# Kernel optimization log

Measured on AMD Instinct MI355X. Metric: run time of the kernel, lower is better.

## Reference

```python
import jax, jax.numpy as jnp
import numpy as np

D_MODEL = 512
NUM_HEADS = 8
DEPTH = D_MODEL // NUM_HEADS
NEG_INF = -1e9


def setup_inputs() -> dict:
    key = jax.random.key(0)
    ks = jax.random.split(key, 12)
    B, S = 4, 2048
    scale = 1.0 / np.sqrt(D_MODEL)
    inp = {
        "q": jax.random.normal(ks[0], (B, S, D_MODEL), jnp.float32),
        "k": jax.random.normal(ks[1], (B, S, D_MODEL), jnp.float32),
        "v": jax.random.normal(ks[2], (B, S, D_MODEL), jnp.float32),
        "mask": jnp.zeros((1, 1, S, S), jnp.float32),
        # Dense layer params (keras Dense = x @ W + b)
        "wq": jax.random.normal(ks[3], (D_MODEL, D_MODEL), jnp.float32) * scale,
        "bq": jnp.zeros((D_MODEL,), jnp.float32),
        "wk": jax.random.normal(ks[4], (D_MODEL, D_MODEL), jnp.float32) * scale,
        "bk": jnp.zeros((D_MODEL,), jnp.float32),
        "wv": jax.random.normal(ks[5], (D_MODEL, D_MODEL), jnp.float32) * scale,
        "bv": jnp.zeros((D_MODEL,), jnp.float32),
        "wo": jax.random.normal(ks[6], (D_MODEL, D_MODEL), jnp.float32) * scale,
        "bo": jnp.zeros((D_MODEL,), jnp.float32),
    }
    return inp


def _split_heads(x):
    # [B, S, D] -> [B, H, S, depth]
    B, S, _ = x.shape
    return x.reshape(B, S, NUM_HEADS, DEPTH).transpose(0, 2, 1, 3)


def reference(q, k, v, mask, wq, bq, wk, bk, wv, bv, wo, bo):
    B, S, _ = q.shape
    qh = _split_heads(q @ wq + bq)  # [B,H,S,depth]
    kh = _split_heads(k @ wk + bk)
    vh = _split_heads(v @ wv + bv)
    logits = jnp.einsum("bhqd,bhkd->bhqk", qh, kh) / jnp.sqrt(
        jnp.asarray(DEPTH, qh.dtype)
    )
    logits = logits + mask * NEG_INF
    attn = jax.nn.softmax(logits, axis=-1)
    out = jnp.einsum("bhqk,bhkd->bhqd", attn, vh)  # [B,H,S,depth]
    out = out.transpose(0, 2, 1, 3).reshape(B, S, D_MODEL)
    return out @ wo + bo
```

## Files before the change

### kernel.cpp

```cpp
#include <hip/hip_runtime.h>
#include <hip/hip_bf16.h>

#define S_LEN 2048
#define DM    512
#define NH    8
#define DH    64

typedef float  f4   __attribute__((ext_vector_type(4)));
typedef float  f16v __attribute__((ext_vector_type(16)));
typedef short  s8v  __attribute__((ext_vector_type(8)));
typedef __bf16 b8v  __attribute__((ext_vector_type(8)));
union F8 { s8v s; b8v b; };
union U4 { unsigned u[4]; s8v s; b8v b; };

typedef __attribute__((address_space(1))) const void gas_t;
typedef __attribute__((address_space(3))) void       las_t;

__device__ __forceinline__ void gl16(const void* g, void* l) {
  __builtin_amdgcn_global_load_lds((gas_t*)g, (las_t*)l, 16, 0, 0);
}

__device__ __forceinline__ ushort f2bf(float x) {
  unsigned u = __float_as_uint(x);
  u += 0x7FFFu + ((u >> 16) & 1u);
  return (ushort)(u >> 16);
}
__device__ __forceinline__ unsigned pk2(float a, float b) {
  union { __hip_bfloat162 h; unsigned u; } cv;
  cv.h = __float22bfloat162_rn(make_float2(a, b));
  return cv.u;
}

__device__ __forceinline__ void plswap(unsigned a, unsigned b,
                                       unsigned& lo, unsigned& hi2) {
#if __has_builtin(__builtin_amdgcn_permlane32_swap)
  auto r = __builtin_amdgcn_permlane32_swap((int)a, (int)b, false, false);
  lo  = (unsigned)r[0];
  hi2 = (unsigned)r[1];
#else
  const bool ish = (threadIdx.x & 32) != 0;
  const unsigned sa = (unsigned)__shfl_xor((int)a, 32);
  const unsigned sb = (unsigned)__shfl_xor((int)b, 32);
  lo  = ish ? sb : a;
  hi2 = ish ? b  : sa;
#endif
}

__global__ void mask_scan(const float* __restrict__ m, int* __restrict__ flag) {
  const int i = blockIdx.x * 256 + threadIdx.x;
  const float4 v = ((const float4*)m)[i];
  const bool nz = (v.x != 0.f) | (v.y != 0.f) | (v.z != 0.f) | (v.w != 0.f);
  if (nz) atomicOr(flag, 1);
}

__global__ void cvt3(const float* __restrict__ q, const float* __restrict__ k,
                     const float* __restrict__ v, ushort* __restrict__ oq,
                     ushort* __restrict__ ok, ushort* __restrict__ ov) {
  const int z = blockIdx.y;
  const float* s = (z == 0) ? q : (z == 1) ? k : v;
  ushort* d = (z == 0) ? oq : (z == 1) ? ok : ov;
  const size_t i = ((size_t)blockIdx.x * 256 + threadIdx.x) * 8;
  const float4 a = *(const float4*)(s + i);
  const float4 b = *(const float4*)(s + i + 4);
  s8v r;
  r[0] = (short)f2bf(a.x); r[1] = (short)f2bf(a.y);
  r[2] = (short)f2bf(a.z); r[3] = (short)f2bf(a.w);
  r[4] = (short)f2bf(b.x); r[5] = (short)f2bf(b.y);
  r[6] = (short)f2bf(b.z); r[7] = (short)f2bf(b.w);
  *(s8v*)(d + i) = r;
}

__global__ void wtrans(const float* __restrict__ w0, const float* __restrict__ w1,
                       const float* __restrict__ w2, const float* __restrict__ w3,
                       ushort* __restrict__ o0, ushort* __restrict__ o1,
                       ushort* __restrict__ o2, ushort* __restrict__ o3) {
  const int z = blockIdx.z;
  const float* src = (z == 0) ? w0 : (z == 1) ? w1 : (z == 2) ? w2 : w3;
  ushort* dst = (z == 0) ? o0 : (z == 1) ? o1 : (z == 2) ? o2 : o3;
  __shared__ float tile[32][33];
  const int tx = threadIdx.x, ty = threadIdx.y;
  const int k0 = blockIdx.x * 32, n0 = blockIdx.y * 32;
#pragma unroll
  for (int i = 0; i < 4; ++i)
    tile[ty + i * 8][tx] = src[(size_t)(k0 + ty + i * 8) * DM + n0 + tx];
  __syncthreads();
#pragma unroll
  for (int i = 0; i < 4; ++i)
    dst[(size_t)(n0 + ty + i * 8) * DM + k0 + tx] = f2bf(tile[tx][ty + i * 8]);
}

__device__ __forceinline__ void gemm_core(
    const ushort* __restrict__ A, const ushort* __restrict__ Bt,
    const float* __restrict__ bias, void* __restrict__ out, int mode,
    ushort* As, ushort* Bs) {
  const int tid  = threadIdx.x;
  const int lane = tid & 63, wave = tid >> 6;
  const int ql = lane & 15, lg = lane >> 4;
  const int wr = wave >> 1, wc = wave & 1;
  const int tm = blockIdx.x, tn = blockIdx.y;

  const int srow  = wave * 32 + (lane >> 2);
  const int sbyte = (lane & 3) * 16;

  const char* gA = (const char*)(A  + (size_t)(tm * 128 + srow) * 512) + sbyte;
  const char* gB = (const char*)(Bt + (size_t)(tn * 128 + srow) * 512) + sbyte;
  char* lA = (char*)As + wave * 2048;
  char* lB = (char*)Bs + wave * 2048;

  f4 acc[4][4] = {};

  for (int kt = 0; kt < 16; ++kt) {
    const size_t gofs = (size_t)kt * 64;
    gl16(gA + gofs, lA);
    gl16(gA + gofs + 16 * 512 * 2, lA + 1024);
    gl16(gB + gofs, lB);
    gl16(gB + gofs + 16 * 512 * 2, lB + 1024);
    __syncthreads();
    F8 af[4], bf[4];
#pragma unroll
    for (int i = 0; i < 4; ++i) {
      af[i].s = *(const s8v*)(As + (wr * 64 + i * 16 + ql) * 32 + lg * 8);
      bf[i].s = *(const s8v*)(Bs + (wc * 64 + i * 16 + ql) * 32 + lg * 8);
    }
#pragma unroll
    for (int i = 0; i < 4; ++i)
#pragma unroll
      for (int j = 0; j < 4; ++j)
        acc[i][j] = __builtin_amdgcn_mfma_f32_16x16x32_bf16(af[i].b, bf[j].b,
                                                            acc[i][j], 0, 0, 0);
    __syncthreads();
  }

#pragma unroll
  for (int i = 0; i < 4; ++i) {
#pragma unroll
    for (int j = 0; j < 4; ++j) {
      const int n = tn * 128 + wc * 64 + j * 16 + ql;
      const float bz = bias[n];
#pragma unroll
      for (int r = 0; r < 4; ++r) {
        const int m = tm * 128 + wr * 64 + i * 16 + lg * 4 + r;
        const float val = acc[i][j][r] + bz;
        if (mode == 2) {
          ((float*)out)[(size_t)m * DM + n] = val;
        } else {
          const int b = m >> 11, s = m & 2047, h = n >> 6, d = n & 63;
          if (mode == 0)
            ((ushort*)out)[((size_t)(b * NH + h) * S_LEN + s) * DH + d] = f2bf(val);
          else
            ((ushort*)out)[((size_t)(b * NH + h) * DH + d) * S_LEN + s] = f2bf(val);
        }
      }
    }
  }
}

__global__ __launch_bounds__(256) void gemm_qkv(
    const ushort* __restrict__ Xq, const ushort* __restrict__ Xk,
    const ushort* __restrict__ Xv, const ushort* __restrict__ Wtq,
    const ushort* __restrict__ Wtk, const ushort* __restrict__ Wtv,
    const float* __restrict__ bq, const float* __restrict__ bk,
    const float* __restrict__ bv, ushort* __restrict__ Qh,
    ushort* __restrict__ Kh, ushort* __restrict__ Vt) {
  __shared__ ushort As[128 * 32], Bs[128 * 32];
  const int z = blockIdx.z;
  const ushort* A  = (z == 0) ? Xq : (z == 1) ? Xk : Xv;
  const ushort* Bp = (z == 0) ? Wtq : (z == 1) ? Wtk : Wtv;
  const float* bias = (z == 0) ? bq : (z == 1) ? bk : bv;
  void* out = (z == 0) ? (void*)Qh : (z == 1) ? (void*)Kh : (void*)Vt;
  gemm_core(A, Bp, bias, out, (z == 2) ? 1 : 0, As, Bs);
}

__global__ __launch_bounds__(256) void gemm_o(
    const ushort* __restrict__ Obf, const ushort* __restrict__ Wto,
    const float* __restrict__ bo, float* __restrict__ out) {
  __shared__ ushort As[128 * 32], Bs[128 * 32];
  gemm_core(Obf, Wto, bo, out, 2, As, Bs);
}

__global__ __launch_bounds__(256, 2) void attn(
    const ushort* __restrict__ Qh, const ushort* __restrict__ Kh,
    const ushort* __restrict__ Vt, const float* __restrict__ mask,
    const int* __restrict__ flagp, ushort* __restrict__ Obf) {
  __shared__ ushort Ks[2][4096];
  __shared__ ushort Vs[2][4096];

  const float K2 = 0.18033688011f;
  const float C2 = 17.3123404907f;

  const int bid = (blockIdx.x & 7) * 64 + (blockIdx.x >> 3);
  const int bh = bid >> 4, qb = bid & 15;
  const int tid = threadIdx.x, lane = tid & 63, wave = tid >> 6;
  const int cl = lane & 31, hi = lane >> 5;
  const int q = qb * 128 + wave * 32 + cl;
  const bool um = (*flagp) != 0;
  const char* KbC = (const char*)(Kh + (size_t)bh * S_LEN * DH);
  const char* VbC = (const char*)(Vt + (size_t)bh * DH * S_LEN);
  const unsigned swz = (unsigned)((cl & 7) << 4);

  int kofs[2], vofs[2];
#pragma unroll
  for (int c = 0; c < 2; ++c) {
    const int ui  = wave * 128 + c * 64 + lane;
    const int row = ui >> 3, u = ui & 7;
    const int xu  = u ^ (row & 7);
    kofs[c] = row * 128  + (xu << 4);
    vofs[c] = row * 4096 + (xu << 4);
  }

  F8 qf[4];
#pragma unroll
  for (int c = 0; c < 4; ++c)
    qf[c].s = *(const s8v*)(Qh + ((size_t)bh * S_LEN + q) * DH + hi * 8 + 16 * c);

  float lrun = 0.f;
  f16v oacc0 = {}, oacc1 = {};

  {
    char* kl = (char*)&Ks[0][0] + wave * 2048;
    char* vl = (char*)&Vs[0][0] + wave * 2048;
    gl16(KbC + kofs[0], kl);
    gl16(KbC + kofs[1], kl + 1024);
    gl16(VbC + vofs[0], vl);
    gl16(VbC + vofs[1], vl + 1024);
  }
  __syncthreads();

  int cur = 0;
  for (int kt = 0; kt < 32; ++kt) {
    if (kt + 1 < 32) {
      const char* kg = KbC + (size_t)(kt + 1) * 8192;
      const char* vg = VbC + (size_t)(kt + 1) * 128;
      char* kl = (char*)&Ks[cur ^ 1][0] + wave * 2048;
      char* vl = (char*)&Vs[cur ^ 1][0] + wave * 2048;
      gl16(kg + kofs[0], kl);
      gl16(kg + kofs[1], kl + 1024);
      gl16(vg + vofs[0], vl);
      gl16(vg + vofs[1], vl + 1024);
    }

    const int kv0 = kt * 64;
    const char* KtB = (const char*)&Ks[cur][0];
    const char* VtB = (const char*)&Vs[cur][0];

    const char* kr0 = KtB + (size_t)cl * 128;
    const char* kr1 = KtB + (size_t)(32 + cl) * 128;
    f16v s0 = {}, s1 = {};
    __builtin_amdgcn_s_setprio(1);
#pragma unroll
    for (int c = 0; c < 4; ++c) {
      const unsigned off = ((unsigned)(hi * 16 + 32 * c)) ^ swz;
      F8 ka0, ka1;
      ka0.s = *(const s8v*)(kr0 + off);
      ka1.s = *(const s8v*)(kr1 + off);
      s0 = __builtin_amdgcn_mfma_f32_32x32x16_bf16(ka0.b, qf[c].b, s0, 0, 0, 0);
      s1 = __builtin_amdgcn_mfma_f32_32x32x16_bf16(ka1.b, qf[c].b, s1, 0, 0, 0);
    }
    __builtin_amdgcn_s_setprio(0);

    if (um) {
#pragma unroll
      for (int r = 0; r < 16; ++r) {
        const int kvr = kv0 + (r & 3) + 8 * (r >> 2) + 4 * hi;
        s0[r] += mask[(size_t)q * S_LEN + kvr] * (-8e9f);
        s1[r] += mask[(size_t)q * S_LEN + kvr + 32] * (-8e9f);
      }
    }

    float pv0[16], pv1[16];
#pragma unroll
    for (int r = 0; r < 16; ++r) {
      pv0[r] = exp2f(fmaf(s0[r], K2, -C2));
      pv1[r] = exp2f(fmaf(s1[r], K2, -C2));
    }
    {
      float t[16];
#pragma unroll
      for (int r = 0; r < 16; ++r) t[r] = pv0[r] + pv1[r];
#pragma unroll
      for (int st = 8; st > 0; st >>= 1)
#pragma unroll
        for (int r = 0; r < st; ++r) t[r] += t[r + st];
      lrun += t[0];
    }

    unsigned P0[4][2], P1[4][2];
#pragma unroll
    for (int u = 0; u < 4; ++u)
#pragma unroll
      for (int e = 0; e < 2; ++e) {
        P0[u][e] = pk2(pv0[4 * u + 2 * e], pv0[4 * u + 2 * e + 1]);
        P1[u][e] = pk2(pv1[4 * u + 2 * e], pv1[4 * u + 2 * e + 1]);
      }
    U4 pf[4];
#pragma unroll
    for (int half = 0; half < 2; ++half)
#pragma unroll
      for (int e = 0; e < 2; ++e) {
        unsigned lo, h2;
        plswap(P0[2 * half][e], P0[2 * half + 1][e], lo, h2);
        pf[half].u[e] = lo; pf[half].u[2 + e] = h2;
        plswap(P1[2 * half][e], P1[2 * half + 1][e], lo, h2);
        pf[2 + half].u[e] = lo; pf[2 + half].u[2 + e] = h2;
      }

    const char* vr0 = VtB + (size_t)cl * 128;
    const char* vr1 = VtB + (size_t)(32 + cl) * 128;
    __builtin_amdgcn_s_setprio(1);
#pragma unroll
    for (int c = 0; c < 4; ++c) {
      const unsigned off = ((unsigned)(hi * 16 + 32 * c)) ^ swz;
      F8 va0, va1;
      va0.s = *(const s8v*)(vr0 + off);
      va1.s = *(const s8v*)(vr1 + off);
      oacc0 = __builtin_amdgcn_mfma_f32_32x32x16_bf16(va0.b, pf[c].b, oacc0, 0, 0, 0);
      oacc1 = __builtin_amdgcn_mfma_f32_32x32x16_bf16(va1.b, pf[c].b, oacc1, 0, 0, 0);
    }
    __builtin_amdgcn_s_setprio(0);

    __syncthreads();
    cur ^= 1;
  }

  const float lt = lrun + __shfl_xor(lrun, 32);
  const float inv = 1.f / lt;
  const int b = bh >> 3, h = bh & 7;
  ushort* op = Obf + ((size_t)(b * S_LEN + q)) * DM + h * DH;
#pragma unroll
  for (int u = 0; u < 4; ++u) {
    const int d0 = 8 * u + 4 * hi;
    *(uint2*)(op + d0) =
        make_uint2(pk2(oacc0[4 * u] * inv, oacc0[4 * u + 1] * inv),
                   pk2(oacc0[4 * u + 2] * inv, oacc0[4 * u + 3] * inv));
    *(uint2*)(op + 32 + d0) =
        make_uint2(pk2(oacc1[4 * u] * inv, oacc1[4 * u + 1] * inv),
                   pk2(oacc1[4 * u + 2] * inv, oacc1[4 * u + 3] * inv));
  }
}

extern "C" void kernel_launch(void* const* d_in, const int* in_sizes, int n_in,
                              void* d_out, int out_size, void* d_ws, size_t ws_size,
                              hipStream_t stream) {
  (void)in_sizes; (void)n_in; (void)out_size; (void)ws_size;
  const float* q    = (const float*)d_in[0];
  const float* k    = (const float*)d_in[1];
  const float* v    = (const float*)d_in[2];
  const float* mask = (const float*)d_in[3];
  const float* wq   = (const float*)d_in[4];
  const float* bq   = (const float*)d_in[5];
  const float* wk   = (const float*)d_in[6];
  const float* bk   = (const float*)d_in[7];
  const float* wv   = (const float*)d_in[8];
  const float* bv   = (const float*)d_in[9];
  const float* wo   = (const float*)d_in[10];
  const float* bo   = (const float*)d_in[11];

  char* ws = (char*)d_ws;
  const size_t SZX = (size_t)8192 * 512 * 2;
  ushort* Xq  = (ushort*)(ws + 0 * SZX);
  ushort* Xk  = (ushort*)(ws + 1 * SZX);
  ushort* Xv  = (ushort*)(ws + 2 * SZX);
  ushort* Qh  = (ushort*)(ws + 3 * SZX);
  ushort* Kh  = (ushort*)(ws + 4 * SZX);
  ushort* Vt  = (ushort*)(ws + 5 * SZX);
  ushort* Obf = Xq;
  const size_t SZW = (size_t)512 * 512 * 2;
  ushort* Wtq = (ushort*)(ws + 6 * SZX + 0 * SZW);
  ushort* Wtk = (ushort*)(ws + 6 * SZX + 1 * SZW);
  ushort* Wtv = (ushort*)(ws + 6 * SZX + 2 * SZW);
  ushort* Wto = (ushort*)(ws + 6 * SZX + 3 * SZW);
  int* flag   = (int*)(ws + 6 * SZX + 4 * SZW);

  hipMemsetAsync(flag, 0, 4, stream);
  mask_scan<<<4096, 256, 0, stream>>>(mask, flag);
  cvt3<<<dim3(2048, 3), 256, 0, stream>>>(q, k, v, Xq, Xk, Xv);
  wtrans<<<dim3(16, 16, 4), dim3(32, 8), 0, stream>>>(wq, wk, wv, wo,
                                                      Wtq, Wtk, Wtv, Wto);
  gemm_qkv<<<dim3(64, 4, 3), 256, 0, stream>>>(Xq, Xk, Xv, Wtq, Wtk, Wtv,
                                               bq, bk, bv, Qh, Kh, Vt);
  attn<<<512, 256, 0, stream>>>(Qh, Kh, Vt, mask, flag, Obf);
  gemm_o<<<dim3(64, 4), 256, 0, stream>>>(Obf, Wto, bo, (float*)d_out);
}
```

Before: 135.6 us.

## Triple-buffer attention K/V tiles, compute row sums via MFMA, fuse mask scan

The attention loop now uses three LDS buffers with a prefetch distance of two tiles and an explicit vmcnt wait plus a single barrier per tile, replacing the double-buffered loop with its trailing __syncthreads. The softmax denominator is accumulated by an extra MFMA against a ones vector instead of a per-lane VALU add tree and a cross-lane shuffle. The mask-scan kernel is folded into the conversion kernel as extra grid rows, which removes one launch. LDS use per block grows by half, which could lower occupancy, and the row sum is now built from bf16-rounded probabilities.

```diff
diff --git a/kernel.cpp b/kernel.cpp
--- a/kernel.cpp
+++ b/kernel.cpp
@@ -46,17 +46,18 @@
 #endif
 }
 
-__global__ void mask_scan(const float* __restrict__ m, int* __restrict__ flag) {
-  const int i = blockIdx.x * 256 + threadIdx.x;
-  const float4 v = ((const float4*)m)[i];
-  const bool nz = (v.x != 0.f) | (v.y != 0.f) | (v.z != 0.f) | (v.w != 0.f);
-  if (nz) atomicOr(flag, 1);
-}
-
-__global__ void cvt3(const float* __restrict__ q, const float* __restrict__ k,
-                     const float* __restrict__ v, ushort* __restrict__ oq,
-                     ushort* __restrict__ ok, ushort* __restrict__ ov) {
+__global__ void cvt_mask(const float* __restrict__ q, const float* __restrict__ k,
+                         const float* __restrict__ v, const float* __restrict__ mask,
+                         ushort* __restrict__ oq, ushort* __restrict__ ok,
+                         ushort* __restrict__ ov, int* __restrict__ flag) {
   const int z = blockIdx.y;
+  if (z >= 3) {
+    const size_t i = (((size_t)(z - 3) * 2048 + blockIdx.x) * 256 + threadIdx.x) * 4;
+    const float4 m4 = *(const float4*)(mask + i);
+    const bool nz = (m4.x != 0.f) | (m4.y != 0.f) | (m4.z != 0.f) | (m4.w != 0.f);
+    if (nz) atomicOr(flag, 1);
+    return;
+  }
   const float* s = (z == 0) ? q : (z == 1) ? k : v;
   ushort* d = (z == 0) ? oq : (z == 1) ? ok : ov;
   const size_t i = ((size_t)blockIdx.x * 256 + threadIdx.x) * 8;
@@ -182,8 +183,8 @@
     const ushort* __restrict__ Qh, const ushort* __restrict__ Kh,
     const ushort* __restrict__ Vt, const float* __restrict__ mask,
     const int* __restrict__ flagp, ushort* __restrict__ Obf) {
-  __shared__ ushort Ks[2][4096];
-  __shared__ ushort Vs[2][4096];
+  __shared__ ushort Ks[3][4096];
+  __shared__ ushort Vs[3][4096];
 
   const float K2 = 0.18033688011f;
   const float C2 = 17.3123404907f;
@@ -213,35 +214,35 @@
   for (int c = 0; c < 4; ++c)
     qf[c].s = *(const s8v*)(Qh + ((size_t)bh * S_LEN + q) * DH + hi * 8 + 16 * c);
 
-  float lrun = 0.f;
-  f16v oacc0 = {}, oacc1 = {};
-
-  {
-    char* kl = (char*)&Ks[0][0] + wave * 2048;
-    char* vl = (char*)&Vs[0][0] + wave * 2048;
-    gl16(KbC + kofs[0], kl);
-    gl16(KbC + kofs[1], kl + 1024);
-    gl16(VbC + vofs[0], vl);
-    gl16(VbC + vofs[1], vl + 1024);
-  }
-  __syncthreads();
-
-  int cur = 0;
-  for (int kt = 0; kt < 32; ++kt) {
-    if (kt + 1 < 32) {
-      const char* kg = KbC + (size_t)(kt + 1) * 8192;
-      const char* vg = VbC + (size_t)(kt + 1) * 128;
-      char* kl = (char*)&Ks[cur ^ 1][0] + wave * 2048;
-      char* vl = (char*)&Vs[cur ^ 1][0] + wave * 2048;
-      gl16(kg + kofs[0], kl);
-      gl16(kg + kofs[1], kl + 1024);
-      gl16(vg + vofs[0], vl);
-      gl16(vg + vofs[1], vl + 1024);
-    }
+  F8 ones;
+#pragma unroll
+  for (int i = 0; i < 8; ++i) ones.s[i] = (short)0x3F80;
+
+  f16v oacc0 = {}, oacc1 = {}, sacc = {};
+
+  auto stage = [&](int kt, int buf) {
+    const char* kg = KbC + (size_t)kt * 8192;
+    const char* vg = VbC + (size_t)kt * 128;
+    char* kl = (char*)&Ks[buf][0] + wave * 2048;
+    char* vl = (char*)&Vs[buf][0] + wave * 2048;
+    gl16(kg + kofs[0], kl);
+    gl16(kg + kofs[1], kl + 1024);
+    gl16(vg + vofs[0], vl);
+    gl16(vg + vofs[1], vl + 1024);
+  };
+
+  stage(0, 0);
+  stage(1, 1);
+
+  auto tile_body = [&](int kt, int rb, int sb, bool last) {
+    if (last) asm volatile("s_waitcnt vmcnt(0)" ::: "memory");
+    else      asm volatile("s_waitcnt vmcnt(4)" ::: "memory");
+    __builtin_amdgcn_s_barrier();
+    if (sb >= 0) stage(kt + 2, sb);
 
     const int kv0 = kt * 64;
-    const char* KtB = (const char*)&Ks[cur][0];
-    const char* VtB = (const char*)&Vs[cur][0];
+    const char* KtB = (const char*)&Ks[rb][0];
+    const char* VtB = (const char*)&Vs[rb][0];
 
     const char* kr0 = KtB + (size_t)cl * 128;
     const char* kr1 = KtB + (size_t)(32 + cl) * 128;
@@ -273,16 +274,6 @@
       pv0[r] = exp2f(fmaf(s0[r], K2, -C2));
       pv1[r] = exp2f(fmaf(s1[r], K2, -C2));
     }
-    {
-      float t[16];
-#pragma unroll
-      for (int r = 0; r < 16; ++r) t[r] = pv0[r] + pv1[r];
-#pragma unroll
-      for (int st = 8; st > 0; st >>= 1)
-#pragma unroll
-        for (int r = 0; r < st; ++r) t[r] += t[r + st];
-      lrun += t[0];
-    }
 
     unsigned P0[4][2], P1[4][2];
 #pragma unroll
@@ -315,15 +306,21 @@
       va1.s = *(const s8v*)(vr1 + off);
       oacc0 = __builtin_amdgcn_mfma_f32_32x32x16_bf16(va0.b, pf[c].b, oacc0, 0, 0, 0);
       oacc1 = __builtin_amdgcn_mfma_f32_32x32x16_bf16(va1.b, pf[c].b, oacc1, 0, 0, 0);
+      sacc  = __builtin_amdgcn_mfma_f32_32x32x16_bf16(ones.b, pf[c].b, sacc, 0, 0, 0);
     }
     __builtin_amdgcn_s_setprio(0);
-
-    __syncthreads();
-    cur ^= 1;
-  }
-
-  const float lt = lrun + __shfl_xor(lrun, 32);
-  const float inv = 1.f / lt;
+  };
+
+#pragma unroll 1
+  for (int g = 0; g < 10; ++g) {
+    tile_body(3 * g,     0, 2, false);
+    tile_body(3 * g + 1, 1, 0, false);
+    tile_body(3 * g + 2, 2, 1, false);
+  }
+  tile_body(30, 0, -1, false);
+  tile_body(31, 1, -1, true);
+
+  const float inv = 1.f / sacc[0];
   const int b = bh >> 3, h = bh & 7;
   ushort* op = Obf + ((size_t)(b * S_LEN + q)) * DM + h * DH;
 #pragma unroll
@@ -372,8 +369,7 @@
   int* flag   = (int*)(ws + 6 * SZX + 4 * SZW);
 
   hipMemsetAsync(flag, 0, 4, stream);
-  mask_scan<<<4096, 256, 0, stream>>>(mask, flag);
-  cvt3<<<dim3(2048, 3), 256, 0, stream>>>(q, k, v, Xq, Xk, Xv);
+  cvt_mask<<<dim3(2048, 5), 256, 0, stream>>>(q, k, v, mask, Xq, Xk, Xv, flag);
   wtrans<<<dim3(16, 16, 4), dim3(32, 8), 0, stream>>>(wq, wk, wv, wo,
                                                       Wtq, Wtk, Wtv, Wto);
   gemm_qkv<<<dim3(64, 4, 3), 256, 0, stream>>>(Xq, Xk, Xv, Wtq, Wtk, Wtv,
```

Measured after the change: 137.1 us. No clear change (+1.1%).

## Merge prep kernels into one launch and halve attention block size

Applied to the files above, without the earlier changes.

Folds the mask scan, the activation bf16 conversion and the weight transpose into a single prep kernel, which removes two kernel launches. The attention kernel moves from 256-thread blocks covering 128 queries to 128-thread blocks covering 64 queries, giving 1024 blocks with launch bounds of 8 per SM. Each wave now stages more of every K/V tile. The smaller blocks aim to improve occupancy and load balance across CUs, at the cost of more K/V traffic because each K/V tile is reloaded for fewer queries.

```diff
diff --git a/kernel.cpp b/kernel.cpp
--- a/kernel.cpp
+++ b/kernel.cpp
@@ -46,17 +46,40 @@
 #endif
 }
 
-__global__ void mask_scan(const float* __restrict__ m, int* __restrict__ flag) {
-  const int i = blockIdx.x * 256 + threadIdx.x;
-  const float4 v = ((const float4*)m)[i];
-  const bool nz = (v.x != 0.f) | (v.y != 0.f) | (v.z != 0.f) | (v.w != 0.f);
-  if (nz) atomicOr(flag, 1);
-}
-
-__global__ void cvt3(const float* __restrict__ q, const float* __restrict__ k,
-                     const float* __restrict__ v, ushort* __restrict__ oq,
-                     ushort* __restrict__ ok, ushort* __restrict__ ov) {
+__global__ void prep(const float* __restrict__ q, const float* __restrict__ k,
+                     const float* __restrict__ v, const float* __restrict__ mask,
+                     const float* __restrict__ w0, const float* __restrict__ w1,
+                     const float* __restrict__ w2, const float* __restrict__ w3,
+                     ushort* __restrict__ oq, ushort* __restrict__ ok,
+                     ushort* __restrict__ ov, ushort* __restrict__ o0,
+                     ushort* __restrict__ o1, ushort* __restrict__ o2,
+                     ushort* __restrict__ o3, int* __restrict__ flag) {
   const int z = blockIdx.y;
+  if (z == 5) {
+    const int bx = blockIdx.x;
+    if (bx >= 1024) return;
+    const int w = bx >> 8;
+    const float* src = (w == 0) ? w0 : (w == 1) ? w1 : (w == 2) ? w2 : w3;
+    ushort* dst = (w == 0) ? o0 : (w == 1) ? o1 : (w == 2) ? o2 : o3;
+    __shared__ float tile[32][33];
+    const int tx = threadIdx.x & 31, ty = threadIdx.x >> 5;
+    const int k0 = (bx & 15) * 32, n0 = ((bx >> 4) & 15) * 32;
+#pragma unroll
+    for (int i = 0; i < 4; ++i)
+      tile[ty + i * 8][tx] = src[(size_t)(k0 + ty + i * 8) * DM + n0 + tx];
+    __syncthreads();
+#pragma unroll
+    for (int i = 0; i < 4; ++i)
+      dst[(size_t)(n0 + ty + i * 8) * DM + k0 + tx] = f2bf(tile[tx][ty + i * 8]);
+    return;
+  }
+  if (z >= 3) {
+    const size_t i = (((size_t)(z - 3) * 2048 + blockIdx.x) * 256 + threadIdx.x) * 4;
+    const float4 m4 = *(const float4*)(mask + i);
+    const bool nz = (m4.x != 0.f) | (m4.y != 0.f) | (m4.z != 0.f) | (m4.w != 0.f);
+    if (nz) atomicOr(flag, 1);
+    return;
+  }
   const float* s = (z == 0) ? q : (z == 1) ? k : v;
   ushort* d = (z == 0) ? oq : (z == 1) ? ok : ov;
   const size_t i = ((size_t)blockIdx.x * 256 + threadIdx.x) * 8;
@@ -68,25 +91,6 @@
   r[4] = (short)f2bf(b.x); r[5] = (short)f2bf(b.y);
   r[6] = (short)f2bf(b.z); r[7] = (short)f2bf(b.w);
   *(s8v*)(d + i) = r;
-}
-
-__global__ void wtrans(const float* __restrict__ w0, const float* __restrict__ w1,
-                       const float* __restrict__ w2, const float* __restrict__ w3,
-                       ushort* __restrict__ o0, ushort* __restrict__ o1,
-                       ushort* __restrict__ o2, ushort* __restrict__ o3) {
-  const int z = blockIdx.z;
-  const float* src = (z == 0) ? w0 : (z == 1) ? w1 : (z == 2) ? w2 : w3;
-  ushort* dst = (z == 0) ? o0 : (z == 1) ? o1 : (z == 2) ? o2 : o3;
-  __shared__ float tile[32][33];
-  const int tx = threadIdx.x, ty = threadIdx.y;
-  const int k0 = blockIdx.x * 32, n0 = blockIdx.y * 32;
-#pragma unroll
-  for (int i = 0; i < 4; ++i)
-    tile[ty + i * 8][tx] = src[(size_t)(k0 + ty + i * 8) * DM + n0 + tx];
-  __syncthreads();
-#pragma unroll
-  for (int i = 0; i < 4; ++i)
-    dst[(size_t)(n0 + ty + i * 8) * DM + k0 + tx] = f2bf(tile[tx][ty + i * 8]);
 }
 
 __device__ __forceinline__ void gemm_core(
@@ -178,7 +182,7 @@
   gemm_core(Obf, Wto, bo, out, 2, As, Bs);
 }
 
-__global__ __launch_bounds__(256, 2) void attn(
+__global__ __launch_bounds__(128, 8) void attn(
     const ushort* __restrict__ Qh, const ushort* __restrict__ Kh,
     const ushort* __restrict__ Vt, const float* __restrict__ mask,
     const int* __restrict__ flagp, ushort* __restrict__ Obf) {
@@ -188,20 +192,20 @@
   const float K2 = 0.18033688011f;
   const float C2 = 17.3123404907f;
 
-  const int bid = (blockIdx.x & 7) * 64 + (blockIdx.x >> 3);
-  const int bh = bid >> 4, qb = bid & 15;
+  const int bid = (blockIdx.x & 7) * 128 + (blockIdx.x >> 3);
+  const int bh = bid >> 5, qb = bid & 31;
   const int tid = threadIdx.x, lane = tid & 63, wave = tid >> 6;
   const int cl = lane & 31, hi = lane >> 5;
-  const int q = qb * 128 + wave * 32 + cl;
+  const int q = qb * 64 + wave * 32 + cl;
   const bool um = (*flagp) != 0;
   const char* KbC = (const char*)(Kh + (size_t)bh * S_LEN * DH);
   const char* VbC = (const char*)(Vt + (size_t)bh * DH * S_LEN);
   const unsigned swz = (unsigned)((cl & 7) << 4);
 
-  int kofs[2], vofs[2];
-#pragma unroll
-  for (int c = 0; c < 2; ++c) {
-    const int ui  = wave * 128 + c * 64 + lane;
+  int kofs[4], vofs[4];
+#pragma unroll
+  for (int c = 0; c < 4; ++c) {
+    const int ui  = c * 128 + wave * 64 + lane;
     const int row = ui >> 3, u = ui & 7;
     const int xu  = u ^ (row & 7);
     kofs[c] = row * 128  + (xu << 4);
@@ -216,28 +220,24 @@
   float lrun = 0.f;
   f16v oacc0 = {}, oacc1 = {};
 
-  {
-    char* kl = (char*)&Ks[0][0] + wave * 2048;
-    char* vl = (char*)&Vs[0][0] + wave * 2048;
-    gl16(KbC + kofs[0], kl);
-    gl16(KbC + kofs[1], kl + 1024);
-    gl16(VbC + vofs[0], vl);
-    gl16(VbC + vofs[1], vl + 1024);
-  }
+  auto stage = [&](int kt, int buf) {
+    const char* kg = KbC + (size_t)kt * 8192;
+    const char* vg = VbC + (size_t)kt * 128;
+    char* kl = (char*)&Ks[buf][0] + (wave * 64) * 16;
+    char* vl = (char*)&Vs[buf][0] + (wave * 64) * 16;
+#pragma unroll
+    for (int c = 0; c < 4; ++c) {
+      gl16(kg + kofs[c], kl + c * 2048);
+      gl16(vg + vofs[c], vl + c * 2048);
+    }
+  };
+
+  stage(0, 0);
   __syncthreads();
 
   int cur = 0;
   for (int kt = 0; kt < 32; ++kt) {
-    if (kt + 1 < 32) {
-      const char* kg = KbC + (size_t)(kt + 1) * 8192;
-      const char* vg = VbC + (size_t)(kt + 1) * 128;
-      char* kl = (char*)&Ks[cur ^ 1][0] + wave * 2048;
-      char* vl = (char*)&Vs[cur ^ 1][0] + wave * 2048;
-      gl16(kg + kofs[0], kl);
-      gl16(kg + kofs[1], kl + 1024);
-      gl16(vg + vofs[0], vl);
-      gl16(vg + vofs[1], vl + 1024);
-    }
+    if (kt + 1 < 32) stage(kt + 1, cur ^ 1);
 
     const int kv0 = kt * 64;
     const char* KtB = (const char*)&Ks[cur][0];
@@ -372,12 +372,10 @@
   int* flag   = (int*)(ws + 6 * SZX + 4 * SZW);
 
   hipMemsetAsync(flag, 0, 4, stream);
-  mask_scan<<<4096, 256, 0, stream>>>(mask, flag);
-  cvt3<<<dim3(2048, 3), 256, 0, stream>>>(q, k, v, Xq, Xk, Xv);
-  wtrans<<<dim3(16, 16, 4), dim3(32, 8), 0, stream>>>(wq, wk, wv, wo,
-                                                      Wtq, Wtk, Wtv, Wto);
+  prep<<<dim3(2048, 6), 256, 0, stream>>>(q, k, v, mask, wq, wk, wv, wo,
+                                          Xq, Xk, Xv, Wtq, Wtk, Wtv, Wto, flag);
   gemm_qkv<<<dim3(64, 4, 3), 256, 0, stream>>>(Xq, Xk, Xv, Wtq, Wtk, Wtv,
                                                bq, bk, bv, Qh, Kh, Vt);
-  attn<<<512, 256, 0, stream>>>(Qh, Kh, Vt, mask, flag, Obf);
+  attn<<<1024, 128, 0, stream>>>(Qh, Kh, Vt, mask, flag, Obf);
   gemm_o<<<dim3(64, 4), 256, 0, stream>>>(Obf, Wto, bo, (float*)d_out);
 }
```

After: 145.4 us. 1.07x slower.
